# Kernel tuning notes

Hardware: AMD Instinct MI355X
Metric: run time of the kernel (lower is better)

## Reference

```python
import jax, jax.numpy as jnp
import numpy as np

K = 31  # AvgPool2d kernel size
P = 15  # padding


def _box_avg(x):
    """31x31 stride-1 avg pool, count_include_pad=True (PyTorch default):
    separable ones-conv with zero padding, divided by K*K."""
    B, C, H, W = x.shape
    kh = jnp.ones((C, 1, K, 1), x.dtype)
    kw = jnp.ones((C, 1, 1, K), x.dtype)
    dn = ('NCHW', 'OIHW', 'NCHW')
    y = jax.lax.conv_general_dilated(x, kh, (1, 1), [(P, P), (0, 0)],
                                     dimension_numbers=dn, feature_group_count=C)
    y = jax.lax.conv_general_dilated(y, kw, (1, 1), [(0, 0), (P, P)],
                                     dimension_numbers=dn, feature_group_count=C)
    return y / (K * K)


def setup_inputs() -> dict:
    key = jax.random.key(0)
    k1, k2 = jax.random.split(key)
    pred = jax.random.normal(k1, (64, 1, 512, 512), dtype=jnp.float32)
    mask = jax.random.uniform(k2, (64, 1, 512, 512), dtype=jnp.float32)
    return {"pred": pred, "mask": mask}


def reference(pred, mask):
    weit = 1.0 + 5.0 * jnp.abs(_box_avg(mask) - mask)
    p = jax.nn.sigmoid(pred)
    inter = jnp.sum(p * mask * weit, axis=(2, 3))          # [B, C]
    union = jnp.sum((p + mask) * weit, axis=(2, 3))        # [B, C]
    wdiss = 1.0 - (2.0 * inter + 0.5) / (union + 0.5)
    return jnp.mean(wdiss)
```

## Files before the change

### kernel.cpp

```cpp
#include <hip/hip_runtime.h>
#include <hip/hip_bf16.h>
#include <math.h>

#define NB 64
#define HH 512
#define WW 512
#define KK 31
#define PP 15
#define NSTRIP 16
#define SROWS (HH / NSTRIP)
#define NROWS (NB * HH)
#define ROWS_PER_WAVE 8

#define WS_NEED (8192 + (size_t)NROWS * WW * 4)

__global__ __launch_bounds__(256) void hrow_kernel(const float* __restrict__ mask,
                                                   float* __restrict__ H) {
    const int gw   = (blockIdx.x * 256 + threadIdx.x) >> 6;
    const int lane = threadIdx.x & 63;

    for (int k = 0; k < ROWS_PER_WAVE; ++k) {
        const size_t r = (size_t)gw * ROWS_PER_WAVE + k;
        const float* row = mask + r * WW;
        const int xbase = lane * 8;
        const float4 a = *(const float4*)(row + xbase);
        const float4 b = *(const float4*)(row + xbase + 4);

        float s0 = a.x;
        float s1 = s0 + a.y;
        float s2 = s1 + a.z;
        float s3 = s2 + a.w;
        float s4 = s3 + b.x;
        float s5 = s4 + b.y;
        float s6 = s5 + b.z;
        float s7 = s6 + b.w;

        float incl = s7;
        #pragma unroll
        for (int off = 1; off < 64; off <<= 1) {
            float t = __shfl_up(incl, off);
            if (lane >= off) incl += t;
        }
        const float base = incl - s7;
        s0 += base; s1 += base; s2 += base; s3 += base;
        s4 += base; s5 += base; s6 += base; s7 += base;

        const float total = __shfl(incl, 63);

        float hi0 = __shfl_down(s7, 1);
        float hi1 = __shfl_down(s0, 2);
        float hi2 = __shfl_down(s1, 2);
        float hi3 = __shfl_down(s2, 2);
        float hi4 = __shfl_down(s3, 2);
        float hi5 = __shfl_down(s4, 2);
        float hi6 = __shfl_down(s5, 2);
        float hi7 = __shfl_down(s6, 2);
        float lo0 = __shfl_up(s0, 2);
        float lo1 = __shfl_up(s1, 2);
        float lo2 = __shfl_up(s2, 2);
        float lo3 = __shfl_up(s3, 2);
        float lo4 = __shfl_up(s4, 2);
        float lo5 = __shfl_up(s5, 2);
        float lo6 = __shfl_up(s6, 2);
        float lo7 = __shfl_up(s7, 2);

        float h[8];
        const float hiv[8] = {hi0, hi1, hi2, hi3, hi4, hi5, hi6, hi7};
        const float lov[8] = {lo0, lo1, lo2, lo3, lo4, lo5, lo6, lo7};
        #pragma unroll
        for (int j = 0; j < 8; ++j) {
            const int x = xbase + j;
            const float mhi = (x + PP > WW - 1) ? total : hiv[j];
            const float mlo = (x - PP - 1 >= 0) ? lov[j] : 0.0f;
            h[j] = mhi - mlo;
        }

        float* orow = H + r * WW;
        *(float4*)(orow + xbase)     = make_float4(h[0], h[1], h[2], h[3]);
        *(float4*)(orow + xbase + 4) = make_float4(h[4], h[5], h[6], h[7]);
    }
}

__global__ __launch_bounds__(512) void dice_kernel(
        const float* __restrict__ pred,
        const float* __restrict__ mask,
        const float* __restrict__ H,
        float* __restrict__ part) {
    const int strip = blockIdx.x;
    const int b     = blockIdx.y;
    const int x     = threadIdx.x;
    const int wave  = x >> 6;
    const int lane  = x & 63;

    __shared__ float red[16];

    const float* Hb = H    + (size_t)b * HH * WW;
    const float* mb = mask + (size_t)b * HH * WW;
    const float* pb = pred + (size_t)b * HH * WW;
    const int y0 = strip * SROWS;

    float B = 0.0f;
    {
        const int rlo = (y0 - PP < 0) ? 0 : y0 - PP;
        const int rhi = y0 + PP - 1;
        for (int r = rlo; r <= rhi; ++r) B += Hb[r * WW + x];
    }

    float inter = 0.0f, uni = 0.0f;
    #pragma unroll 4
    for (int i = 0; i < SROWS; ++i) {
        const int y = y0 + i;
        const float he = (y + PP < HH) ? Hb[(y + PP) * WW + x] : 0.0f;
        const float hl = (y - PP >= 0) ? Hb[(y - PP) * WW + x] : 0.0f;
        const float m  = mb[y * WW + x];
        const float p  = pb[y * WW + x];
        B += he;
        const float avg = B * (1.0f / (float)(KK * KK));
        const float w   = 1.0f + 5.0f * fabsf(avg - m);
        const float sg  = 1.0f / (1.0f + __expf(-p));
        inter += sg * m * w;
        uni   += (sg + m) * w;
        B -= hl;
    }

    #pragma unroll
    for (int off = 32; off > 0; off >>= 1) {
        inter += __shfl_down(inter, off);
        uni   += __shfl_down(uni, off);
    }
    if (lane == 0) { red[wave] = inter; red[8 + wave] = uni; }
    __syncthreads();
    if (x == 0) {
        float ti = 0.0f, tu = 0.0f;
        #pragma unroll
        for (int w2 = 0; w2 < 8; ++w2) { ti += red[w2]; tu += red[8 + w2]; }
        const int bid = b * NSTRIP + strip;
        part[bid] = ti;
        part[NB * NSTRIP + bid] = tu;
    }
}

#define RPB 4
#define NROUND (SROWS / RPB)
#define PSTR 544

__global__ __launch_bounds__(512, 8) void dice_strip_kernel(
        const float* __restrict__ pred,
        const float* __restrict__ mask,
        float* __restrict__ part) {
    const int strip = blockIdx.x;
    const int b     = blockIdx.y;
    const int x     = threadIdx.x;
    const int wave  = x >> 6;
    const int lane  = x & 63;

    __shared__ float wtot[RPB * 8];
    __shared__ float Pbuf[RPB * PSTR];
    __shared__ float red[16];

    const float* mbase = mask + (size_t)b * HH * WW;
    const float* pbase = pred + (size_t)b * HH * WW;
    const int y0 = strip * SROWS;

    if (x < 16) {
        #pragma unroll
        for (int r = 0; r < RPB; ++r) Pbuf[r * PSTR + x] = 0.0f;
    }

    float vcarry = 0.0f;
    {
        const int rlo = (y0 - PP - 1 < 0) ? 0 : y0 - PP - 1;
        const int rhi = (y0 + PP - 1 > HH - 1) ? HH - 1 : y0 + PP - 1;
        for (int r = rlo; r <= rhi; ++r) vcarry += mbase[r * WW + x];
    }

    float inter = 0.0f, uni = 0.0f;

    for (int j = 0; j < NROUND; ++j) {
        const int y = y0 + j * RPB;
        float en[RPB], lv[RPB], mc[RPB], pv[RPB];
        #pragma unroll
        for (int r = 0; r < RPB; ++r) {
            const int ra = y + r + PP;
            const int rs = y + r - PP - 1;
            en[r] = (ra < HH) ? mbase[ra * WW + x] : 0.0f;
            lv[r] = (rs >= 0) ? mbase[rs * WW + x] : 0.0f;
            mc[r] = mbase[(y + r) * WW + x];
            pv[r] = pbase[(y + r) * WW + x];
        }
        float incl[RPB];
        {
            float run = vcarry;
            #pragma unroll
            for (int r = 0; r < RPB; ++r) { run += en[r] - lv[r]; incl[r] = run; }
            vcarry = run;
        }
        #pragma unroll
        for (int off = 1; off < 64; off <<= 1) {
            float t[RPB];
            #pragma unroll
            for (int r = 0; r < RPB; ++r) t[r] = __shfl_up(incl[r], off);
            #pragma unroll
            for (int r = 0; r < RPB; ++r) if (lane >= off) incl[r] += t[r];
        }
        if (lane == 63) {
            #pragma unroll
            for (int r = 0; r < RPB; ++r) wtot[r * 8 + wave] = incl[r];
        }
        __syncthreads();
        float bm[RPB];
        #pragma unroll
        for (int r = 0; r < RPB; ++r) bm[r] = (lane < wave) ? wtot[r * 8 + lane] : 0.0f;
        #pragma unroll
        for (int off = 1; off < 64; off <<= 1) {
            #pragma unroll
            for (int r = 0; r < RPB; ++r) bm[r] += __shfl_xor(bm[r], off);
        }
        #pragma unroll
        for (int r = 0; r < RPB; ++r) Pbuf[r * PSTR + 16 + x] = bm[r] + incl[r];
        if (wave == 7) {
            #pragma unroll
            for (int r = 0; r < RPB; ++r) {
                const float p511 = bm[r] + wtot[r * 8 + 7];
                if (lane >= 48) Pbuf[r * PSTR + 528 + (lane - 48)] = p511;
            }
        }
        __syncthreads();
        #pragma unroll
        for (int r = 0; r < RPB; ++r) {
            const float hsum = Pbuf[r * PSTR + 16 + x + PP] - Pbuf[r * PSTR + x];
            const float avg  = hsum * (1.0f / (float)(KK * KK));
            const float m    = mc[r];
            const float w    = 1.0f + 5.0f * fabsf(avg - m);
            const float sg   = 1.0f / (1.0f + __expf(-pv[r]));
            inter += sg * m * w;
            uni   += (sg + m) * w;
        }
    }

    #pragma unroll
    for (int off = 32; off > 0; off >>= 1) {
        inter += __shfl_down(inter, off);
        uni   += __shfl_down(uni, off);
    }
    if (lane == 0) { red[wave] = inter; red[8 + wave] = uni; }
    __syncthreads();
    if (x == 0) {
        float ti = 0.0f, tu = 0.0f;
        #pragma unroll
        for (int w2 = 0; w2 < 8; ++w2) { ti += red[w2]; tu += red[8 + w2]; }
        const int bid = b * NSTRIP + strip;
        part[bid] = ti;
        part[NB * NSTRIP + bid] = tu;
    }
}

__global__ void dice_final_kernel(const float* __restrict__ part,
                                  float* __restrict__ out) {
    const int t = threadIdx.x;
    float inter = 0.0f, uni = 0.0f;
    #pragma unroll
    for (int s = 0; s < NSTRIP; ++s) {
        inter += part[t * NSTRIP + s];
        uni   += part[NB * NSTRIP + t * NSTRIP + s];
    }
    float wd = 1.0f - (2.0f * inter + 0.5f) / (uni + 0.5f);
    #pragma unroll
    for (int off = 32; off > 0; off >>= 1) wd += __shfl_down(wd, off);
    if (t == 0) out[0] = wd * (1.0f / (float)NB);
}

extern "C" void kernel_launch(void* const* d_in, const int* in_sizes, int n_in,
                              void* d_out, int out_size, void* d_ws, size_t ws_size,
                              hipStream_t stream) {
    const float* pred = (const float*)d_in[0];
    const float* mask = (const float*)d_in[1];
    float* out  = (float*)d_out;
    float* part = (float*)d_ws;
    float* H    = (float*)((char*)d_ws + 8192);

    dim3 grid2(NSTRIP, NB);
    if (ws_size >= WS_NEED) {
        hrow_kernel<<<1024, 256, 0, stream>>>(mask, H);
        dice_kernel<<<grid2, 512, 0, stream>>>(pred, mask, H, part);
    } else {
        dice_strip_kernel<<<grid2, 512, 0, stream>>>(pred, mask, part);
    }
    dice_final_kernel<<<1, 64, 0, stream>>>(part, out);
}
```

Before: 180.7 us.

## Store horizontal box sums in fp16 and vectorize dice kernel to float4 columns

The intermediate horizontal 31-wide row sums are now written as fp16 instead of fp32, halving the write and re-read traffic of the workspace buffer. The dice kernel is restructured so each thread handles four adjacent columns with vector loads, using 256-thread blocks where each block covers two 32-row strips. Storing sums of up to 31 values in fp16 loses precision (roughly 3 significant digits), which could perturb the weights slightly. The final reduction kernel now takes the partial count and stride as parameters.

New measurement: 189.3 us. +4.7%, slower.

```diff
diff --git a/kernel.cpp b/kernel.cpp
--- a/kernel.cpp
+++ b/kernel.cpp
@@ -7,15 +7,17 @@
 #define WW 512
 #define KK 31
 #define PP 15
-#define NSTRIP 16
-#define SROWS (HH / NSTRIP)
 #define NROWS (NB * HH)
 #define ROWS_PER_WAVE 8
 
-#define WS_NEED (8192 + (size_t)NROWS * WW * 4)
+typedef _Float16 f16;
+typedef f16 f16x8 __attribute__((ext_vector_type(8)));
+typedef f16 f16x4 __attribute__((ext_vector_type(4)));
+
+#define WS_NEED (8192 + (size_t)NROWS * WW * 2)
 
 __global__ __launch_bounds__(256) void hrow_kernel(const float* __restrict__ mask,
-                                                   float* __restrict__ H) {
+                                                   f16* __restrict__ H) {
     const int gw   = (blockIdx.x * 256 + threadIdx.x) >> 6;
     const int lane = threadIdx.x & 63;
 
@@ -47,99 +49,124 @@
 
         const float total = __shfl(incl, 63);
 
-        float hi0 = __shfl_down(s7, 1);
-        float hi1 = __shfl_down(s0, 2);
-        float hi2 = __shfl_down(s1, 2);
-        float hi3 = __shfl_down(s2, 2);
-        float hi4 = __shfl_down(s3, 2);
-        float hi5 = __shfl_down(s4, 2);
-        float hi6 = __shfl_down(s5, 2);
-        float hi7 = __shfl_down(s6, 2);
-        float lo0 = __shfl_up(s0, 2);
-        float lo1 = __shfl_up(s1, 2);
-        float lo2 = __shfl_up(s2, 2);
-        float lo3 = __shfl_up(s3, 2);
-        float lo4 = __shfl_up(s4, 2);
-        float lo5 = __shfl_up(s5, 2);
-        float lo6 = __shfl_up(s6, 2);
-        float lo7 = __shfl_up(s7, 2);
-
-        float h[8];
-        const float hiv[8] = {hi0, hi1, hi2, hi3, hi4, hi5, hi6, hi7};
-        const float lov[8] = {lo0, lo1, lo2, lo3, lo4, lo5, lo6, lo7};
+        float hiv[8], lov[8];
+        hiv[0] = __shfl_down(s7, 1);
+        hiv[1] = __shfl_down(s0, 2);
+        hiv[2] = __shfl_down(s1, 2);
+        hiv[3] = __shfl_down(s2, 2);
+        hiv[4] = __shfl_down(s3, 2);
+        hiv[5] = __shfl_down(s4, 2);
+        hiv[6] = __shfl_down(s5, 2);
+        hiv[7] = __shfl_down(s6, 2);
+        lov[0] = __shfl_up(s0, 2);
+        lov[1] = __shfl_up(s1, 2);
+        lov[2] = __shfl_up(s2, 2);
+        lov[3] = __shfl_up(s3, 2);
+        lov[4] = __shfl_up(s4, 2);
+        lov[5] = __shfl_up(s5, 2);
+        lov[6] = __shfl_up(s6, 2);
+        lov[7] = __shfl_up(s7, 2);
+
+        f16x8 hv;
         #pragma unroll
         for (int j = 0; j < 8; ++j) {
             const int x = xbase + j;
             const float mhi = (x + PP > WW - 1) ? total : hiv[j];
             const float mlo = (x - PP - 1 >= 0) ? lov[j] : 0.0f;
-            h[j] = mhi - mlo;
-        }
-
-        float* orow = H + r * WW;
-        *(float4*)(orow + xbase)     = make_float4(h[0], h[1], h[2], h[3]);
-        *(float4*)(orow + xbase + 4) = make_float4(h[4], h[5], h[6], h[7]);
-    }
-}
-
-__global__ __launch_bounds__(512) void dice_kernel(
+            hv[j] = (f16)(mhi - mlo);
+        }
+        *(f16x8*)(H + r * WW + xbase) = hv;
+    }
+}
+
+__device__ inline float4 loadH4(const f16* p) {
+    const f16x4 v = *(const f16x4*)p;
+    return make_float4((float)v[0], (float)v[1], (float)v[2], (float)v[3]);
+}
+
+__global__ __launch_bounds__(256) void dice_kernel(
         const float* __restrict__ pred,
         const float* __restrict__ mask,
-        const float* __restrict__ H,
+        const f16* __restrict__ H,
         float* __restrict__ part) {
-    const int strip = blockIdx.x;
-    const int b     = blockIdx.y;
-    const int x     = threadIdx.x;
-    const int wave  = x >> 6;
-    const int lane  = x & 63;
-
-    __shared__ float red[16];
-
-    const float* Hb = H    + (size_t)b * HH * WW;
+    const int bx   = blockIdx.x;
+    const int b    = blockIdx.y;
+    const int t    = threadIdx.x;
+    const int g    = t >> 7;
+    const int q    = t & 127;
+    const int c    = q * 4;
+    const int wave = t >> 6;
+    const int lane = t & 63;
+
+    __shared__ float red[8];
+
+    const f16*   Hb = H    + (size_t)b * HH * WW;
     const float* mb = mask + (size_t)b * HH * WW;
     const float* pb = pred + (size_t)b * HH * WW;
-    const int y0 = strip * SROWS;
-
-    float B = 0.0f;
+    const int y0 = (bx * 2 + g) * 32;
+
+    float4 B = make_float4(0.f, 0.f, 0.f, 0.f);
     {
         const int rlo = (y0 - PP < 0) ? 0 : y0 - PP;
         const int rhi = y0 + PP - 1;
-        for (int r = rlo; r <= rhi; ++r) B += Hb[r * WW + x];
-    }
-
-    float inter = 0.0f, uni = 0.0f;
+        for (int r = rlo; r <= rhi; ++r) {
+            const float4 h = loadH4(Hb + (size_t)r * WW + c);
+            B.x += h.x; B.y += h.y; B.z += h.z; B.w += h.w;
+        }
+    }
+
+    float4 inter4 = make_float4(0.f, 0.f, 0.f, 0.f);
+    float4 uni4   = make_float4(0.f, 0.f, 0.f, 0.f);
+    const float4 zero4 = make_float4(0.f, 0.f, 0.f, 0.f);
+    const float inv2 = 1.0f / (float)(KK * KK);
+
     #pragma unroll 4
-    for (int i = 0; i < SROWS; ++i) {
+    for (int i = 0; i < 32; ++i) {
         const int y = y0 + i;
-        const float he = (y + PP < HH) ? Hb[(y + PP) * WW + x] : 0.0f;
-        const float hl = (y - PP >= 0) ? Hb[(y - PP) * WW + x] : 0.0f;
-        const float m  = mb[y * WW + x];
-        const float p  = pb[y * WW + x];
-        B += he;
-        const float avg = B * (1.0f / (float)(KK * KK));
-        const float w   = 1.0f + 5.0f * fabsf(avg - m);
-        const float sg  = 1.0f / (1.0f + __expf(-p));
-        inter += sg * m * w;
-        uni   += (sg + m) * w;
-        B -= hl;
-    }
-
+        const float4 he = (y + PP < HH) ? loadH4(Hb + (size_t)(y + PP) * WW + c) : zero4;
+        const float4 hl = (y - PP >= 0) ? loadH4(Hb + (size_t)(y - PP) * WW + c) : zero4;
+        const float4 m  = *(const float4*)(mb + (size_t)y * WW + c);
+        const float4 p  = *(const float4*)(pb + (size_t)y * WW + c);
+
+        B.x += he.x; B.y += he.y; B.z += he.z; B.w += he.w;
+
+        const float w0 = 1.0f + 5.0f * fabsf(B.x * inv2 - m.x);
+        const float w1 = 1.0f + 5.0f * fabsf(B.y * inv2 - m.y);
+        const float w2 = 1.0f + 5.0f * fabsf(B.z * inv2 - m.z);
+        const float w3 = 1.0f + 5.0f * fabsf(B.w * inv2 - m.w);
+        const float sg0 = 1.0f / (1.0f + __expf(-p.x));
+        const float sg1 = 1.0f / (1.0f + __expf(-p.y));
+        const float sg2 = 1.0f / (1.0f + __expf(-p.z));
+        const float sg3 = 1.0f / (1.0f + __expf(-p.w));
+
+        inter4.x += sg0 * m.x * w0;  uni4.x += (sg0 + m.x) * w0;
+        inter4.y += sg1 * m.y * w1;  uni4.y += (sg1 + m.y) * w1;
+        inter4.z += sg2 * m.z * w2;  uni4.z += (sg2 + m.z) * w2;
+        inter4.w += sg3 * m.w * w3;  uni4.w += (sg3 + m.w) * w3;
+
+        B.x -= hl.x; B.y -= hl.y; B.z -= hl.z; B.w -= hl.w;
+    }
+
+    float inter = inter4.x + inter4.y + inter4.z + inter4.w;
+    float uni   = uni4.x + uni4.y + uni4.z + uni4.w;
     #pragma unroll
     for (int off = 32; off > 0; off >>= 1) {
         inter += __shfl_down(inter, off);
         uni   += __shfl_down(uni, off);
     }
-    if (lane == 0) { red[wave] = inter; red[8 + wave] = uni; }
+    if (lane == 0) { red[wave] = inter; red[4 + wave] = uni; }
     __syncthreads();
-    if (x == 0) {
-        float ti = 0.0f, tu = 0.0f;
-        #pragma unroll
-        for (int w2 = 0; w2 < 8; ++w2) { ti += red[w2]; tu += red[8 + w2]; }
-        const int bid = b * NSTRIP + strip;
-        part[bid] = ti;
-        part[NB * NSTRIP + bid] = tu;
-    }
-}
-
+    if (t == 0) {
+        const float ti = red[0] + red[1] + red[2] + red[3];
+        const float tu = red[4] + red[5] + red[6] + red[7];
+        const int bid = b * 8 + bx;
+        part[bid]       = ti;
+        part[512 + bid] = tu;
+    }
+}
+
+#define NSTRIP 16
+#define SROWS (HH / NSTRIP)
 #define RPB 4
 #define NROUND (SROWS / RPB)
 #define PSTR 544
@@ -166,16 +193,13 @@
         #pragma unroll
         for (int r = 0; r < RPB; ++r) Pbuf[r * PSTR + x] = 0.0f;
     }
-
     float vcarry = 0.0f;
     {
         const int rlo = (y0 - PP - 1 < 0) ? 0 : y0 - PP - 1;
         const int rhi = (y0 + PP - 1 > HH - 1) ? HH - 1 : y0 + PP - 1;
         for (int r = rlo; r <= rhi; ++r) vcarry += mbase[r * WW + x];
     }
-
     float inter = 0.0f, uni = 0.0f;
-
     for (int j = 0; j < NROUND; ++j) {
         const int y = y0 + j * RPB;
         float en[RPB], lv[RPB], mc[RPB], pv[RPB];
@@ -197,11 +221,11 @@
         }
         #pragma unroll
         for (int off = 1; off < 64; off <<= 1) {
-            float t[RPB];
-            #pragma unroll
-            for (int r = 0; r < RPB; ++r) t[r] = __shfl_up(incl[r], off);
-            #pragma unroll
-            for (int r = 0; r < RPB; ++r) if (lane >= off) incl[r] += t[r];
+            float tt[RPB];
+            #pragma unroll
+            for (int r = 0; r < RPB; ++r) tt[r] = __shfl_up(incl[r], off);
+            #pragma unroll
+            for (int r = 0; r < RPB; ++r) if (lane >= off) incl[r] += tt[r];
         }
         if (lane == 63) {
             #pragma unroll
@@ -237,7 +261,6 @@
             uni   += (sg + m) * w;
         }
     }
-
     #pragma unroll
     for (int off = 32; off > 0; off >>= 1) {
         inter += __shfl_down(inter, off);
@@ -256,13 +279,12 @@
 }
 
 __global__ void dice_final_kernel(const float* __restrict__ part,
-                                  float* __restrict__ out) {
+                                  float* __restrict__ out, int nper, int stride) {
     const int t = threadIdx.x;
     float inter = 0.0f, uni = 0.0f;
-    #pragma unroll
-    for (int s = 0; s < NSTRIP; ++s) {
-        inter += part[t * NSTRIP + s];
-        uni   += part[NB * NSTRIP + t * NSTRIP + s];
+    for (int s = 0; s < nper; ++s) {
+        inter += part[t * nper + s];
+        uni   += part[stride + t * nper + s];
     }
     float wd = 1.0f - (2.0f * inter + 0.5f) / (uni + 0.5f);
     #pragma unroll
@@ -277,14 +299,16 @@
     const float* mask = (const float*)d_in[1];
     float* out  = (float*)d_out;
     float* part = (float*)d_ws;
-    float* H    = (float*)((char*)d_ws + 8192);
-
-    dim3 grid2(NSTRIP, NB);
+    f16*   H    = (f16*)((char*)d_ws + 8192);
+
     if (ws_size >= WS_NEED) {
         hrow_kernel<<<1024, 256, 0, stream>>>(mask, H);
-        dice_kernel<<<grid2, 512, 0, stream>>>(pred, mask, H, part);
+        dim3 grid2(8, NB);
+        dice_kernel<<<grid2, 256, 0, stream>>>(pred, mask, H, part);
+        dice_final_kernel<<<1, 64, 0, stream>>>(part, out, 8, 512);
     } else {
+        dim3 grid2(NSTRIP, NB);
         dice_strip_kernel<<<grid2, 512, 0, stream>>>(pred, mask, part);
-    }
-    dice_final_kernel<<<1, 64, 0, stream>>>(part, out);
-}
+        dice_final_kernel<<<1, 64, 0, stream>>>(part, out, NSTRIP, NB * NSTRIP);
+    }
+}
```
